# Kernel tuning notes

Hardware: AMD Instinct MI355X
Metric: run time of the kernel (lower is better)

The kernel has to match this reference:

```python
import jax, jax.numpy as jnp
import numpy as np

N = 100000
E = 1600000
DIN = 128
DOUT = 128
NUM_STEPS = 3


def setup_inputs() -> dict:
    key = jax.random.key(0)
    ks = jax.random.split(key, 12)
    stdv = 1.0 / np.sqrt(DOUT)
    xav = np.sqrt(6.0 / (2 * DOUT + DOUT))  # xavier_uniform for [DOUT, 2*DOUT]
    return {
        "input": jax.random.normal(ks[0], (N, DIN), dtype=jnp.float32),
        "edge_row": jax.random.randint(ks[1], (E,), 0, N, dtype=jnp.int32),
        "edge_col": jax.random.randint(ks[2], (E,), 0, N, dtype=jnp.int32),
        "edge_weight": jax.random.uniform(ks[3], (E,), dtype=jnp.float32),
        "weight": jax.random.uniform(ks[4], (DIN, DOUT), jnp.float32, -stdv, stdv),
        "bias": jax.random.uniform(ks[5], (DOUT,), jnp.float32, -stdv, stdv),
        "candidate_weight": jax.random.uniform(ks[6], (DOUT, DOUT), jnp.float32, -stdv, stdv),
        "ug_W": jax.random.uniform(ks[7], (DOUT, 2 * DOUT), jnp.float32, -xav, xav),
        "ug_b": jnp.zeros((DOUT,), jnp.float32),
        "rg_W": jax.random.uniform(ks[8], (DOUT, 2 * DOUT), jnp.float32, -xav, xav),
        "rg_b": jnp.zeros((DOUT,), jnp.float32),
    }


def reference(input, edge_row, edge_col, edge_weight, weight, bias,
              candidate_weight, ug_W, ug_b, rg_W, rg_b):
    n = input.shape[0]
    # h = input @ W + b
    h = input @ weight + bias
    for _ in range(NUM_STEPS):
        # spmm: m[dst] += w_e * h[src]
        msg = edge_weight[:, None] * h[edge_col]          # [E, DOUT]
        m = jax.ops.segment_sum(msg, edge_row, num_segments=n)  # [N, DOUT]
        g = jnp.concatenate([h, m], axis=1)               # [N, 2*DOUT]
        z = jax.nn.sigmoid(g @ ug_W.T + ug_b)
        r = jax.nn.sigmoid(g @ rg_W.T + rg_b)
        cand = jnp.tanh((r * h) @ candidate_weight)
        h = z * h + (1.0 - z) * cand
    return h
```

## Files before the change

kernel.cpp:

```cpp
#include <hip/hip_runtime.h>
#include <math.h>

#define NN 100000
#define EE 1600000
#define D 128
#define NB 782
#define SBLK 392
#define EPB 4096
#define EMAX 2048

typedef __attribute__((ext_vector_type(8))) short short8;
typedef __attribute__((ext_vector_type(4))) float floatx4;

static __device__ __forceinline__ unsigned short f2bf(float f) {
  unsigned int u = __builtin_bit_cast(unsigned int, f);
  u = (u + 0x7fff + ((u >> 16) & 1)) >> 16;
  return (unsigned short)u;
}
static __device__ __forceinline__ unsigned int pk2(float a, float b) {
  return (unsigned int)f2bf(a) | ((unsigned int)f2bf(b) << 16);
}
static __device__ __forceinline__ float bflo(unsigned int u) { return __builtin_bit_cast(float, u << 16); }
static __device__ __forceinline__ float bfhi(unsigned int u) { return __builtin_bit_cast(float, u & 0xffff0000u); }
static __device__ __forceinline__ float bf2f(unsigned short s) {
  return __builtin_bit_cast(float, (unsigned int)s << 16);
}
static __device__ __forceinline__ float sig_f(float x) { return 1.f / (1.f + __expf(-x)); }
static __device__ __forceinline__ float tanh_f(float x) {
  float e = __expf(2.f * x);
  return 1.f - 2.f / (e + 1.f);
}
static __device__ __forceinline__ void fma8(float* acc, float w, uint4 h) {
  acc[0] += w * bflo(h.x); acc[1] += w * bfhi(h.x);
  acc[2] += w * bflo(h.y); acc[3] += w * bfhi(h.y);
  acc[4] += w * bflo(h.z); acc[5] += w * bfhi(h.z);
  acc[6] += w * bflo(h.w); acc[7] += w * bfhi(h.w);
}


__global__ __launch_bounds__(256) void b_count(const int* __restrict__ erow, int* __restrict__ cnt_pb) {
  __shared__ int s[NB];
  const int tid = threadIdx.x;
  for (int b = tid; b < NB; b += 256) s[b] = 0;
  __syncthreads();
  const int base = blockIdx.x * EPB;
#pragma unroll
  for (int i = 0; i < 16; ++i) {
    int idx = base + i * 256 + tid;
    if (idx < EE) atomicAdd(&s[erow[idx] >> 7], 1);
  }
  __syncthreads();
  for (int b = tid; b < NB; b += 256) cnt_pb[blockIdx.x * NB + b] = s[b];
}

__global__ __launch_bounds__(1024) void b_scan(const int* __restrict__ cnt_pb,
                                               int* __restrict__ base_pb, int* __restrict__ bucket_off) {
  __shared__ int s[1024];
  const int b = threadIdx.x;
  int tot = 0;
  if (b < NB) {
    for (int j = 0; j < SBLK; ++j) tot += cnt_pb[j * NB + b];
  }
  s[b] = tot;
  __syncthreads();
  for (int d = 1; d < 1024; d <<= 1) {
    int v = (b >= d) ? s[b - d] : 0;
    __syncthreads();
    s[b] += v;
    __syncthreads();
  }
  int excl = s[b] - tot;
  if (b < NB) {
    bucket_off[b] = excl;
    int run = excl;
    for (int j = 0; j < SBLK; ++j) { base_pb[j * NB + b] = run; run += cnt_pb[j * NB + b]; }
  }
  if (b == NB - 1) bucket_off[NB] = excl + tot;
}

__global__ __launch_bounds__(256) void b_scatter(const int* __restrict__ erow, const int* __restrict__ ecol,
                                                  const float* __restrict__ ew,
                                                  const int* __restrict__ base_pb, int2* __restrict__ arena) {
  __shared__ int cur[NB];
  const int tid = threadIdx.x;
  for (int b = tid; b < NB; b += 256) cur[b] = base_pb[blockIdx.x * NB + b];
  __syncthreads();
  const int base = blockIdx.x * EPB;
#pragma unroll
  for (int i = 0; i < 16; ++i) {
    int idx = base + i * 256 + tid;
    if (idx < EE) {
      int r = erow[idx];
      int pos = atomicAdd(&cur[r >> 7], 1);
      int2 v;
      v.x = ecol[idx] | ((r & 127) << 24);
      v.y = __builtin_bit_cast(int, ew[idx]);
      arena[pos] = v;
    }
  }
}

__global__ __launch_bounds__(256) void b_sort(const int* __restrict__ bucket_off, const int2* __restrict__ arena,
                                              int2* __restrict__ edata, int* __restrict__ row_start) {
  __shared__ int rcnt[128];
  __shared__ int rcur[128];
  const int b = blockIdx.x;
  const int tid = threadIdx.x;
  const int lo = bucket_off[b], hi = bucket_off[b + 1];

  if (tid < 128) rcnt[tid] = 0;
  __syncthreads();
  for (int i = lo + tid; i < hi; i += 256) atomicAdd(&rcnt[(arena[i].x >> 24) & 127], 1);
  __syncthreads();
  int myc = (tid < 128) ? rcnt[tid] : 0;
  for (int d = 1; d < 128; d <<= 1) {
    int v = (tid < 128 && tid >= d) ? rcnt[tid - d] : 0;
    __syncthreads();
    if (tid < 128) rcnt[tid] += v;
    __syncthreads();
  }
  if (tid < 128) {
    int excl = rcnt[tid] - myc;
    rcur[tid] = lo + excl;
    int gr = b * 128 + tid;
    if (gr < NN) row_start[gr] = lo + excl;
  }
  if (b == NB - 1 && tid == 0) row_start[NN] = hi;
  __syncthreads();

  for (int i = lo + tid; i < hi; i += 256) {
    int2 v = arena[i];
    int rl = (v.x >> 24) & 127;
    int pos = atomicAdd(&rcur[rl], 1);
    int2 o;
    o.x = v.x & 0x00FFFFFF;
    o.y = v.y;
    edata[pos] = o;
  }
}

__global__ __launch_bounds__(64) void k_pack_zr(const float* __restrict__ ugW, const float* __restrict__ rgW,
                                                unsigned int* __restrict__ packZR) {
  int g = blockIdx.x;
  int nt = g >> 3, ks = g & 7;
  int lane = threadIdx.x;
  int o = nt * 16 + (lane & 15);
  int c0 = ks * 32 + (lane >> 4) * 8;
  const float* src = (o < 128 ? ugW + (size_t)o * 256 : rgW + (size_t)(o - 128) * 256) + c0;
  float4 f0 = ((const float4*)src)[0];
  float4 f1 = ((const float4*)src)[1];
  uint4 out;
  out.x = pk2(f0.x, f0.y);
  out.y = pk2(f0.z, f0.w);
  out.z = pk2(f1.x, f1.y);
  out.w = pk2(f1.z, f1.w);
  ((uint4*)packZR)[g * 64 + lane] = out;
}

__global__ __launch_bounds__(64) void k_pack_kn(const float* __restrict__ M, unsigned int* __restrict__ pack) {
  int g = blockIdx.x;
  int nt = g >> 2, ks = g & 3;
  int lane = threadIdx.x;
  int n = nt * 16 + (lane & 15);
  int k0 = ks * 32 + (lane >> 4) * 8;
  unsigned short v[8];
#pragma unroll
  for (int j = 0; j < 8; ++j) v[j] = f2bf(M[(size_t)(k0 + j) * 128 + n]);
  uint4 out;
  out.x = (unsigned int)v[0] | ((unsigned int)v[1] << 16);
  out.y = (unsigned int)v[2] | ((unsigned int)v[3] << 16);
  out.z = (unsigned int)v[4] | ((unsigned int)v[5] << 16);
  out.w = (unsigned int)v[6] | ((unsigned int)v[7] << 16);
  ((uint4*)pack)[g * 64 + lane] = out;
}

__global__ __launch_bounds__(256) void init_mfma(
    const float* __restrict__ X, const short* __restrict__ packW, const float* __restrict__ bias,
    unsigned short* __restrict__ h_bf) {
  __shared__ __align__(16) short sX[32 * 136];
  const int tid = threadIdx.x;
  const int row0 = blockIdx.x * 32;

  {
    int r = tid >> 3, ch = tid & 7;
    const float4* px = (const float4*)(X + (size_t)(row0 + r) * D + ch * 16);
    float4 f0 = px[0], f1 = px[1], f2 = px[2], f3 = px[3];
    uint4 o0, o1;
    o0.x = pk2(f0.x, f0.y); o0.y = pk2(f0.z, f0.w);
    o0.z = pk2(f1.x, f1.y); o0.w = pk2(f1.z, f1.w);
    o1.x = pk2(f2.x, f2.y); o1.y = pk2(f2.z, f2.w);
    o1.z = pk2(f3.x, f3.y); o1.w = pk2(f3.z, f3.w);
    *(uint4*)(sX + r * 136 + ch * 16) = o0;
    *(uint4*)(sX + r * 136 + ch * 16 + 8) = o1;
  }
  __syncthreads();

  const int wave = tid >> 6, lane = tid & 63;
  const int quad = lane >> 4, l15 = lane & 15;
  const int mh = wave & 1, nh = wave >> 1;
  const int mrow = mh * 16 + l15;

  floatx4 acc[4];
  const floatx4 zero4 = {0.f, 0.f, 0.f, 0.f};
#pragma unroll
  for (int t = 0; t < 4; ++t) acc[t] = zero4;

  const short8* pW = (const short8*)packW;
#pragma unroll
  for (int ks = 0; ks < 4; ++ks) {
    short8 a = *(const short8*)(sX + mrow * 136 + ks * 32 + quad * 8);
#pragma unroll
    for (int t = 0; t < 4; ++t) {
      short8 b = pW[((nh * 4 + t) * 4 + ks) * 64 + lane];
      acc[t] = __builtin_amdgcn_mfma_f32_16x16x32_bf16(a, b, acc[t], 0, 0, 0);
    }
  }

  __syncthreads();
#pragma unroll
  for (int t = 0; t < 4; ++t) {
    int col = nh * 64 + t * 16 + l15;
    float bv = bias[col];
#pragma unroll
    for (int reg = 0; reg < 4; ++reg) {
      int row = mh * 16 + quad * 4 + reg;
      sX[row * 136 + col] = (short)f2bf(acc[t][reg] + bv);
    }
  }
  __syncthreads();
  for (int idx = tid; idx < 512; idx += 256) {
    int r = idx >> 4, ch = idx & 15;
    *(uint4*)(h_bf + (size_t)(row0 + r) * D + ch * 8) = *(uint4*)(sX + r * 136 + ch * 8);
  }
}

__global__ __launch_bounds__(512, 8) void fused_step(
    const int* __restrict__ row_start, const int2* __restrict__ edata,
    const uint4* __restrict__ h4,
    const short* __restrict__ packZR, const short* __restrict__ packCW,
    const float* __restrict__ ugb, const float* __restrict__ rgb,
    unsigned short* __restrict__ h_bf_out, float* __restrict__ h_f32_out, int last) {
  __shared__ __align__(16) short sA[32 * 264];
  __shared__ __align__(16) char sU[EMAX * 8];
  int2* sE = (int2*)sU;
  short* sRH = (short*)sU;

  const int tid = threadIdx.x;
  const int row0 = blockIdx.x * 32;
  const int wave = tid >> 6, lane = tid & 63;
  const int sub = lane >> 4, li = lane & 15;

  {
    int r = tid >> 4, ch = tid & 15;
    *(uint4*)(sA + r * 264 + ch * 8) = h4[(size_t)(row0 + r) * 16 + ch];
  }

  const int myrow = row0 + wave * 4 + sub;
  const int rs0 = row_start[myrow];
  const int rs1 = row_start[myrow + 1];
  const int seg_lo = row_start[row0];
  const int seg_hi = row_start[row0 + 32];

  float acc[8];
#pragma unroll
  for (int j = 0; j < 8; ++j) acc[j] = 0.f;

  for (int clo = seg_lo; clo < seg_hi; clo += EMAX) {
    const int chi = min(clo + EMAX, seg_hi);
    for (int i = clo + tid; i < chi; i += 512) sE[i - clo] = edata[i];
    __syncthreads();

    int kb = max(rs0, clo) - clo;
    int ke = min(rs1, chi) - clo;
    for (; kb + 2 <= ke; kb += 2) {
      int2 e0 = sE[kb];
      int2 e1 = sE[kb + 1];
      uint4 h0 = h4[(size_t)e0.x * 16 + li];
      uint4 h1 = h4[(size_t)e1.x * 16 + li];
      fma8(acc, __builtin_bit_cast(float, e0.y), h0);
      fma8(acc, __builtin_bit_cast(float, e1.y), h1);
    }
    if (kb < ke) {
      int2 e0 = sE[kb];
      uint4 h0 = h4[(size_t)e0.x * 16 + li];
      fma8(acc, __builtin_bit_cast(float, e0.y), h0);
    }
    __syncthreads();
  }

  {
    uint4 o;
    o.x = pk2(acc[0], acc[1]);
    o.y = pk2(acc[2], acc[3]);
    o.z = pk2(acc[4], acc[5]);
    o.w = pk2(acc[6], acc[7]);
    *(uint4*)(sA + (wave * 4 + sub) * 264 + 128 + li * 8) = o;
  }
  __syncthreads();

  const int quad = lane >> 4, l15 = lane & 15;
  const int mh = wave >> 2, nh = wave & 3;
  const int mrow = mh * 16 + l15;

  floatx4 accZ[2], accR[2];
  const floatx4 zero4 = {0.f, 0.f, 0.f, 0.f};
#pragma unroll
  for (int t = 0; t < 2; ++t) { accZ[t] = zero4; accR[t] = zero4; }

  const short8* pB = (const short8*)packZR;
#pragma unroll
  for (int ks = 0; ks < 8; ++ks) {
    short8 a = *(const short8*)(sA + mrow * 264 + ks * 32 + quad * 8);
#pragma unroll
    for (int t = 0; t < 2; ++t) {
      short8 bz = pB[((nh * 2 + t) * 8 + ks) * 64 + lane];
      accZ[t] = __builtin_amdgcn_mfma_f32_16x16x32_bf16(a, bz, accZ[t], 0, 0, 0);
      short8 br = pB[((8 + nh * 2 + t) * 8 + ks) * 64 + lane];
      accR[t] = __builtin_amdgcn_mfma_f32_16x16x32_bf16(a, br, accR[t], 0, 0, 0);
    }
  }

#pragma unroll
  for (int t = 0; t < 2; ++t) {
    int col = nh * 32 + t * 16 + l15;
    float zb = ugb[col], rb = rgb[col];
#pragma unroll
    for (int reg = 0; reg < 4; ++reg) {
      int row = mh * 16 + quad * 4 + reg;
      float z = sig_f(accZ[t][reg] + zb);
      float rr = sig_f(accR[t][reg] + rb);
      float hv = bf2f((unsigned short)sA[row * 264 + col]);
      sRH[row * 136 + col] = (short)f2bf(rr * hv);
      accZ[t][reg] = z;
    }
  }
  __syncthreads();

  floatx4 acc2[2];
#pragma unroll
  for (int t = 0; t < 2; ++t) acc2[t] = zero4;

  const short8* pC = (const short8*)packCW;
#pragma unroll
  for (int ks = 0; ks < 4; ++ks) {
    short8 a = *(const short8*)(sRH + mrow * 136 + ks * 32 + quad * 8);
#pragma unroll
    for (int t = 0; t < 2; ++t) {
      short8 b = pC[((nh * 2 + t) * 4 + ks) * 64 + lane];
      acc2[t] = __builtin_amdgcn_mfma_f32_16x16x32_bf16(a, b, acc2[t], 0, 0, 0);
    }
  }

#pragma unroll
  for (int t = 0; t < 2; ++t) {
    int col = nh * 32 + t * 16 + l15;
#pragma unroll
    for (int reg = 0; reg < 4; ++reg) {
      int row = mh * 16 + quad * 4 + reg;
      float cand = tanh_f(acc2[t][reg]);
      float z = accZ[t][reg];
      float hold = bf2f((unsigned short)sA[row * 264 + col]);
      float hn = z * hold + (1.f - z) * cand;
      if (last) h_f32_out[(size_t)(row0 + row) * D + col] = hn;
      else sA[row * 264 + col] = (short)f2bf(hn);
    }
  }
  if (!last) {
    __syncthreads();
    int r = tid >> 4, ch = tid & 15;
    *(uint4*)(h_bf_out + (size_t)(row0 + r) * D + ch * 8) = *(uint4*)(sA + r * 264 + ch * 8);
  }
}

extern "C" void kernel_launch(void* const* d_in, const int* in_sizes, int n_in,
                              void* d_out, int out_size, void* d_ws, size_t ws_size,
                              hipStream_t stream) {
  const float* input = (const float*)d_in[0];
  const int* erow    = (const int*)d_in[1];
  const int* ecol    = (const int*)d_in[2];
  const float* ew    = (const float*)d_in[3];
  const float* W     = (const float*)d_in[4];
  const float* bias  = (const float*)d_in[5];
  const float* CW    = (const float*)d_in[6];
  const float* ugW   = (const float*)d_in[7];
  const float* ugb   = (const float*)d_in[8];
  const float* rgW   = (const float*)d_in[9];
  const float* rgb   = (const float*)d_in[10];

  float* h_out = (float*)d_out;

  char* ws = (char*)d_ws;
  unsigned short* hA = (unsigned short*)ws;   ws += (size_t)NN * D * 2;
  unsigned short* hB = (unsigned short*)ws;   ws += (size_t)NN * D * 2;
  unsigned int* packZR = (unsigned int*)ws;   ws += 16 * 8 * 64 * 16;
  unsigned int* packCW = (unsigned int*)ws;   ws += 8 * 4 * 64 * 16;
  unsigned int* packW  = (unsigned int*)ws;   ws += 8 * 4 * 64 * 16;
  int2* arena    = (int2*)ws;                 ws += (size_t)EE * sizeof(int2);
  int2* edata    = (int2*)ws;                 ws += (size_t)EE * sizeof(int2);
  int* bucket_off= (int*)ws;                  ws += (NB + 1) * sizeof(int);
  int* row_start = (int*)ws;                  ws += (NN + 1) * sizeof(int);
  int* cnt_pb  = (int*)hA;
  int* base_pb = (int*)((char*)hA + (size_t)SBLK * NB * sizeof(int));

  b_count<<<SBLK, 256, 0, stream>>>(erow, cnt_pb);
  b_scan<<<1, 1024, 0, stream>>>(cnt_pb, base_pb, bucket_off);
  b_scatter<<<SBLK, 256, 0, stream>>>(erow, ecol, ew, base_pb, arena);
  b_sort<<<NB, 256, 0, stream>>>(bucket_off, arena, edata, row_start);

  k_pack_zr<<<128, 64, 0, stream>>>(ugW, rgW, packZR);
  k_pack_kn<<<32, 64, 0, stream>>>(CW, packCW);
  k_pack_kn<<<32, 64, 0, stream>>>(W, packW);
  init_mfma<<<NN / 32, 256, 0, stream>>>(input, (const short*)packW, bias, hA);

  fused_step<<<NN / 32, 512, 0, stream>>>(row_start, edata, (const uint4*)hA,
                                          (const short*)packZR, (const short*)packCW,
                                          ugb, rgb, hB, h_out, 0);
  fused_step<<<NN / 32, 512, 0, stream>>>(row_start, edata, (const uint4*)hB,
                                          (const short*)packZR, (const short*)packCW,
                                          ugb, rgb, hA, h_out, 0);
  fused_step<<<NN / 32, 512, 0, stream>>>(row_start, edata, (const uint4*)hA,
                                          (const short*)packZR, (const short*)packCW,
                                          ugb, rgb, hB, h_out, 1);
}
```

Baseline: 530.3 us.

## Replace two-level bucket sort CSR build with global atomic count/scan/scatter

Builds the CSR from edges by counting per row with global atomics, a three-stage scan, and scattering edges directly with per-row atomic cursors. This removes the bucket arena pass and the per-bucket local sort kernel, and the three weight-packing kernels are merged into one launch. In exchange, global atomics now contend on 100k rows, and the edge order within each row becomes nondeterministic. That changes the floating-point summation order and gives a less coalesced scatter.

```diff
diff --git a/kernel.cpp b/kernel.cpp
--- a/kernel.cpp
+++ b/kernel.cpp
@@ -4,9 +4,6 @@
 #define NN 100000
 #define EE 1600000
 #define D 128
-#define NB 782
-#define SBLK 392
-#define EPB 4096
 #define EMAX 2048
 
 typedef __attribute__((ext_vector_type(8))) short short8;
@@ -38,140 +35,106 @@
 }
 
 
-__global__ __launch_bounds__(256) void b_count(const int* __restrict__ erow, int* __restrict__ cnt_pb) {
-  __shared__ int s[NB];
-  const int tid = threadIdx.x;
-  for (int b = tid; b < NB; b += 256) s[b] = 0;
-  __syncthreads();
-  const int base = blockIdx.x * EPB;
-#pragma unroll
-  for (int i = 0; i < 16; ++i) {
-    int idx = base + i * 256 + tid;
-    if (idx < EE) atomicAdd(&s[erow[idx] >> 7], 1);
-  }
-  __syncthreads();
-  for (int b = tid; b < NB; b += 256) cnt_pb[blockIdx.x * NB + b] = s[b];
-}
-
-__global__ __launch_bounds__(1024) void b_scan(const int* __restrict__ cnt_pb,
-                                               int* __restrict__ base_pb, int* __restrict__ bucket_off) {
+__global__ __launch_bounds__(256) void r_count(const int* __restrict__ erow, int* __restrict__ cnt) {
+  int idx = blockIdx.x * 256 + threadIdx.x;
+  if (idx < EE) atomicAdd(&cnt[erow[idx]], 1);
+}
+
+__global__ __launch_bounds__(1024) void r_scan1(const int* __restrict__ cnt,
+                                                int* __restrict__ row_start, int* __restrict__ bsum) {
   __shared__ int s[1024];
-  const int b = threadIdx.x;
-  int tot = 0;
-  if (b < NB) {
-    for (int j = 0; j < SBLK; ++j) tot += cnt_pb[j * NB + b];
-  }
-  s[b] = tot;
+  const int t = threadIdx.x;
+  const int idx = blockIdx.x * 1024 + t;
+  int v = (idx < NN) ? cnt[idx] : 0;
+  s[t] = v;
   __syncthreads();
   for (int d = 1; d < 1024; d <<= 1) {
-    int v = (b >= d) ? s[b - d] : 0;
-    __syncthreads();
-    s[b] += v;
-    __syncthreads();
-  }
-  int excl = s[b] - tot;
-  if (b < NB) {
-    bucket_off[b] = excl;
-    int run = excl;
-    for (int j = 0; j < SBLK; ++j) { base_pb[j * NB + b] = run; run += cnt_pb[j * NB + b]; }
-  }
-  if (b == NB - 1) bucket_off[NB] = excl + tot;
-}
-
-__global__ __launch_bounds__(256) void b_scatter(const int* __restrict__ erow, const int* __restrict__ ecol,
-                                                  const float* __restrict__ ew,
-                                                  const int* __restrict__ base_pb, int2* __restrict__ arena) {
-  __shared__ int cur[NB];
-  const int tid = threadIdx.x;
-  for (int b = tid; b < NB; b += 256) cur[b] = base_pb[blockIdx.x * NB + b];
-  __syncthreads();
-  const int base = blockIdx.x * EPB;
-#pragma unroll
-  for (int i = 0; i < 16; ++i) {
-    int idx = base + i * 256 + tid;
-    if (idx < EE) {
-      int r = erow[idx];
-      int pos = atomicAdd(&cur[r >> 7], 1);
-      int2 v;
-      v.x = ecol[idx] | ((r & 127) << 24);
-      v.y = __builtin_bit_cast(int, ew[idx]);
-      arena[pos] = v;
-    }
-  }
-}
-
-__global__ __launch_bounds__(256) void b_sort(const int* __restrict__ bucket_off, const int2* __restrict__ arena,
-                                              int2* __restrict__ edata, int* __restrict__ row_start) {
-  __shared__ int rcnt[128];
-  __shared__ int rcur[128];
-  const int b = blockIdx.x;
-  const int tid = threadIdx.x;
-  const int lo = bucket_off[b], hi = bucket_off[b + 1];
-
-  if (tid < 128) rcnt[tid] = 0;
-  __syncthreads();
-  for (int i = lo + tid; i < hi; i += 256) atomicAdd(&rcnt[(arena[i].x >> 24) & 127], 1);
-  __syncthreads();
-  int myc = (tid < 128) ? rcnt[tid] : 0;
+    int x = (t >= d) ? s[t - d] : 0;
+    __syncthreads();
+    s[t] += x;
+    __syncthreads();
+  }
+  if (idx < NN) row_start[idx] = s[t] - v;
+  if (t == 1023) bsum[blockIdx.x] = s[1023];
+}
+
+__global__ __launch_bounds__(128) void r_scan2(int* __restrict__ bsum) {
+  __shared__ int s[128];
+  const int t = threadIdx.x;
+  int v = (t < 98) ? bsum[t] : 0;
+  s[t] = v;
+  __syncthreads();
   for (int d = 1; d < 128; d <<= 1) {
-    int v = (tid < 128 && tid >= d) ? rcnt[tid - d] : 0;
-    __syncthreads();
-    if (tid < 128) rcnt[tid] += v;
-    __syncthreads();
-  }
-  if (tid < 128) {
-    int excl = rcnt[tid] - myc;
-    rcur[tid] = lo + excl;
-    int gr = b * 128 + tid;
-    if (gr < NN) row_start[gr] = lo + excl;
-  }
-  if (b == NB - 1 && tid == 0) row_start[NN] = hi;
-  __syncthreads();
-
-  for (int i = lo + tid; i < hi; i += 256) {
-    int2 v = arena[i];
-    int rl = (v.x >> 24) & 127;
-    int pos = atomicAdd(&rcur[rl], 1);
-    int2 o;
-    o.x = v.x & 0x00FFFFFF;
-    o.y = v.y;
-    edata[pos] = o;
-  }
-}
-
-__global__ __launch_bounds__(64) void k_pack_zr(const float* __restrict__ ugW, const float* __restrict__ rgW,
-                                                unsigned int* __restrict__ packZR) {
-  int g = blockIdx.x;
-  int nt = g >> 3, ks = g & 7;
+    int x = (t >= d) ? s[t - d] : 0;
+    __syncthreads();
+    s[t] += x;
+    __syncthreads();
+  }
+  if (t < 98) bsum[t] = s[t] - v;
+}
+
+__global__ __launch_bounds__(1024) void r_scan3(int* __restrict__ row_start, int* __restrict__ row_cur,
+                                                const int* __restrict__ bsum) {
+  const int idx = blockIdx.x * 1024 + threadIdx.x;
+  if (idx < NN) {
+    int v = row_start[idx] + bsum[blockIdx.x];
+    row_start[idx] = v;
+    row_cur[idx] = v;
+  }
+  if (blockIdx.x == 0 && threadIdx.x == 0) row_start[NN] = EE;
+}
+
+__global__ __launch_bounds__(256) void r_scatter(const int* __restrict__ erow, const int* __restrict__ ecol,
+                                                 const float* __restrict__ ew,
+                                                 int* __restrict__ row_cur, int2* __restrict__ edata) {
+  int idx = blockIdx.x * 256 + threadIdx.x;
+  if (idx < EE) {
+    int r = erow[idx];
+    int pos = atomicAdd(&row_cur[r], 1);
+    int2 v;
+    v.x = ecol[idx];
+    v.y = __builtin_bit_cast(int, ew[idx]);
+    edata[pos] = v;
+  }
+}
+
+__global__ __launch_bounds__(64) void k_pack_all(const float* __restrict__ ugW, const float* __restrict__ rgW,
+                                                 const float* __restrict__ CW, const float* __restrict__ W,
+                                                 unsigned int* __restrict__ packZR,
+                                                 unsigned int* __restrict__ packCW,
+                                                 unsigned int* __restrict__ packW) {
   int lane = threadIdx.x;
-  int o = nt * 16 + (lane & 15);
-  int c0 = ks * 32 + (lane >> 4) * 8;
-  const float* src = (o < 128 ? ugW + (size_t)o * 256 : rgW + (size_t)(o - 128) * 256) + c0;
-  float4 f0 = ((const float4*)src)[0];
-  float4 f1 = ((const float4*)src)[1];
-  uint4 out;
-  out.x = pk2(f0.x, f0.y);
-  out.y = pk2(f0.z, f0.w);
-  out.z = pk2(f1.x, f1.y);
-  out.w = pk2(f1.z, f1.w);
-  ((uint4*)packZR)[g * 64 + lane] = out;
-}
-
-__global__ __launch_bounds__(64) void k_pack_kn(const float* __restrict__ M, unsigned int* __restrict__ pack) {
-  int g = blockIdx.x;
-  int nt = g >> 2, ks = g & 3;
-  int lane = threadIdx.x;
-  int n = nt * 16 + (lane & 15);
-  int k0 = ks * 32 + (lane >> 4) * 8;
-  unsigned short v[8];
-#pragma unroll
-  for (int j = 0; j < 8; ++j) v[j] = f2bf(M[(size_t)(k0 + j) * 128 + n]);
-  uint4 out;
-  out.x = (unsigned int)v[0] | ((unsigned int)v[1] << 16);
-  out.y = (unsigned int)v[2] | ((unsigned int)v[3] << 16);
-  out.z = (unsigned int)v[4] | ((unsigned int)v[5] << 16);
-  out.w = (unsigned int)v[6] | ((unsigned int)v[7] << 16);
-  ((uint4*)pack)[g * 64 + lane] = out;
+  if (blockIdx.x < 128) {
+    int g = blockIdx.x;
+    int nt = g >> 3, ks = g & 7;
+    int o = nt * 16 + (lane & 15);
+    int c0 = ks * 32 + (lane >> 4) * 8;
+    const float* src = (o < 128 ? ugW + (size_t)o * 256 : rgW + (size_t)(o - 128) * 256) + c0;
+    float4 f0 = ((const float4*)src)[0];
+    float4 f1 = ((const float4*)src)[1];
+    uint4 out;
+    out.x = pk2(f0.x, f0.y);
+    out.y = pk2(f0.z, f0.w);
+    out.z = pk2(f1.x, f1.y);
+    out.w = pk2(f1.z, f1.w);
+    ((uint4*)packZR)[g * 64 + lane] = out;
+  } else {
+    const float* M = (blockIdx.x < 160) ? CW : W;
+    unsigned int* dst = (blockIdx.x < 160) ? packCW : packW;
+    int g = (blockIdx.x - 128) & 31;
+    int nt = g >> 2, ks = g & 3;
+    int n = nt * 16 + (lane & 15);
+    int k0 = ks * 32 + (lane >> 4) * 8;
+    unsigned short v[8];
+#pragma unroll
+    for (int j = 0; j < 8; ++j) v[j] = f2bf(M[(size_t)(k0 + j) * 128 + n]);
+    uint4 out;
+    out.x = (unsigned int)v[0] | ((unsigned int)v[1] << 16);
+    out.y = (unsigned int)v[2] | ((unsigned int)v[3] << 16);
+    out.z = (unsigned int)v[4] | ((unsigned int)v[5] << 16);
+    out.w = (unsigned int)v[6] | ((unsigned int)v[7] << 16);
+    ((uint4*)dst)[g * 64 + lane] = out;
+  }
 }
 
 __global__ __launch_bounds__(256) void init_mfma(
@@ -395,21 +358,20 @@
   unsigned int* packZR = (unsigned int*)ws;   ws += 16 * 8 * 64 * 16;
   unsigned int* packCW = (unsigned int*)ws;   ws += 8 * 4 * 64 * 16;
   unsigned int* packW  = (unsigned int*)ws;   ws += 8 * 4 * 64 * 16;
-  int2* arena    = (int2*)ws;                 ws += (size_t)EE * sizeof(int2);
   int2* edata    = (int2*)ws;                 ws += (size_t)EE * sizeof(int2);
-  int* bucket_off= (int*)ws;                  ws += (NB + 1) * sizeof(int);
+  int* row_cnt   = (int*)ws;                  ws += NN * sizeof(int);
   int* row_start = (int*)ws;                  ws += (NN + 1) * sizeof(int);
-  int* cnt_pb  = (int*)hA;
-  int* base_pb = (int*)((char*)hA + (size_t)SBLK * NB * sizeof(int));
-
-  b_count<<<SBLK, 256, 0, stream>>>(erow, cnt_pb);
-  b_scan<<<1, 1024, 0, stream>>>(cnt_pb, base_pb, bucket_off);
-  b_scatter<<<SBLK, 256, 0, stream>>>(erow, ecol, ew, base_pb, arena);
-  b_sort<<<NB, 256, 0, stream>>>(bucket_off, arena, edata, row_start);
-
-  k_pack_zr<<<128, 64, 0, stream>>>(ugW, rgW, packZR);
-  k_pack_kn<<<32, 64, 0, stream>>>(CW, packCW);
-  k_pack_kn<<<32, 64, 0, stream>>>(W, packW);
+  int* row_cur   = (int*)ws;                  ws += NN * sizeof(int);
+  int* bsum      = (int*)ws;                  ws += 128 * sizeof(int);
+
+  hipMemsetAsync(row_cnt, 0, (size_t)NN * sizeof(int), stream);
+  r_count<<<(EE + 255) / 256, 256, 0, stream>>>(erow, row_cnt);
+  r_scan1<<<98, 1024, 0, stream>>>(row_cnt, row_start, bsum);
+  r_scan2<<<1, 128, 0, stream>>>(bsum);
+  r_scan3<<<98, 1024, 0, stream>>>(row_start, row_cur, bsum);
+  r_scatter<<<(EE + 255) / 256, 256, 0, stream>>>(erow, ecol, ew, row_cur, edata);
+
+  k_pack_all<<<192, 64, 0, stream>>>(ugW, rgW, CW, W, packZR, packCW, packW);
   init_mfma<<<NN / 32, 256, 0, stream>>>(input, (const short*)packW, bias, hA);
 
   fused_step<<<NN / 32, 512, 0, stream>>>(row_start, edata, (const uint4*)hA,
```

Result: slower. 617.6 us (+16.5%).

## Replace per-block bucket scan with global atomic bucket counts and merge pack kernels

Applied to the files above, without the earlier changes.

The edge bucketing preprocessing now uses global atomics for per-bucket totals instead of a per-block count matrix. That removes the single-block scan's serial loops over 392 blocks per bucket. Scatter blocks reserve their ranges with one atomic per bucket, after a local count in shared memory. Larger 1024-thread blocks now cover 16K edges each, and the three weight-pack kernels are merged into a single launch. In exchange the order of edges within a bucket depends on atomics, so floating-point summation order is not deterministic, and a memset launch is added.

```diff
diff --git a/kernel.cpp b/kernel.cpp
--- a/kernel.cpp
+++ b/kernel.cpp
@@ -4,9 +4,9 @@
 #define NN 100000
 #define EE 1600000
 #define D 128
-#define NB 782
-#define SBLK 392
-#define EPB 4096
+#define NBK 782
+#define SBLK 98
+#define EPB 16384
 #define EMAX 2048
 
 typedef __attribute__((ext_vector_type(8))) short short8;
@@ -38,62 +38,67 @@
 }
 
 
-__global__ __launch_bounds__(256) void b_count(const int* __restrict__ erow, int* __restrict__ cnt_pb) {
-  __shared__ int s[NB];
+__global__ __launch_bounds__(1024) void b_count(const int* __restrict__ erow, int* __restrict__ bucket_tot) {
+  __shared__ int s[NBK];
   const int tid = threadIdx.x;
-  for (int b = tid; b < NB; b += 256) s[b] = 0;
+  for (int b = tid; b < NBK; b += 1024) s[b] = 0;
   __syncthreads();
   const int base = blockIdx.x * EPB;
 #pragma unroll
   for (int i = 0; i < 16; ++i) {
-    int idx = base + i * 256 + tid;
+    int idx = base + i * 1024 + tid;
     if (idx < EE) atomicAdd(&s[erow[idx] >> 7], 1);
   }
   __syncthreads();
-  for (int b = tid; b < NB; b += 256) cnt_pb[blockIdx.x * NB + b] = s[b];
-}
-
-__global__ __launch_bounds__(1024) void b_scan(const int* __restrict__ cnt_pb,
-                                               int* __restrict__ base_pb, int* __restrict__ bucket_off) {
+  for (int b = tid; b < NBK; b += 1024) if (s[b]) atomicAdd(&bucket_tot[b], s[b]);
+}
+
+__global__ __launch_bounds__(1024) void b_off(const int* __restrict__ bucket_tot,
+                                              int* __restrict__ bucket_off, int* __restrict__ bucket_cur) {
   __shared__ int s[1024];
-  const int b = threadIdx.x;
-  int tot = 0;
-  if (b < NB) {
-    for (int j = 0; j < SBLK; ++j) tot += cnt_pb[j * NB + b];
-  }
-  s[b] = tot;
+  const int t = threadIdx.x;
+  int v = (t < NBK) ? bucket_tot[t] : 0;
+  s[t] = v;
   __syncthreads();
   for (int d = 1; d < 1024; d <<= 1) {
-    int v = (b >= d) ? s[b - d] : 0;
-    __syncthreads();
-    s[b] += v;
-    __syncthreads();
-  }
-  int excl = s[b] - tot;
-  if (b < NB) {
-    bucket_off[b] = excl;
-    int run = excl;
-    for (int j = 0; j < SBLK; ++j) { base_pb[j * NB + b] = run; run += cnt_pb[j * NB + b]; }
-  }
-  if (b == NB - 1) bucket_off[NB] = excl + tot;
-}
-
-__global__ __launch_bounds__(256) void b_scatter(const int* __restrict__ erow, const int* __restrict__ ecol,
+    int x = (t >= d) ? s[t - d] : 0;
+    __syncthreads();
+    s[t] += x;
+    __syncthreads();
+  }
+  int excl = s[t] - v;
+  if (t < NBK) { bucket_off[t] = excl; bucket_cur[t] = excl; }
+  if (t == NBK - 1) bucket_off[NBK] = excl + v;
+}
+
+__global__ __launch_bounds__(1024) void b_scatter(const int* __restrict__ erow, const int* __restrict__ ecol,
                                                   const float* __restrict__ ew,
-                                                  const int* __restrict__ base_pb, int2* __restrict__ arena) {
-  __shared__ int cur[NB];
+                                                  int* __restrict__ bucket_cur, int2* __restrict__ arena) {
+  __shared__ int cur[NBK];
   const int tid = threadIdx.x;
-  for (int b = tid; b < NB; b += 256) cur[b] = base_pb[blockIdx.x * NB + b];
+  for (int b = tid; b < NBK; b += 1024) cur[b] = 0;
   __syncthreads();
   const int base = blockIdx.x * EPB;
+  int r[16];
 #pragma unroll
   for (int i = 0; i < 16; ++i) {
-    int idx = base + i * 256 + tid;
-    if (idx < EE) {
-      int r = erow[idx];
-      int pos = atomicAdd(&cur[r >> 7], 1);
+    int idx = base + i * 1024 + tid;
+    r[i] = (idx < EE) ? erow[idx] : -1;
+    if (r[i] >= 0) atomicAdd(&cur[r[i] >> 7], 1);
+  }
+  __syncthreads();
+  for (int b = tid; b < NBK; b += 1024) {
+    int c = cur[b];
+    cur[b] = c ? atomicAdd(&bucket_cur[b], c) : 0;
+  }
+  __syncthreads();
+#pragma unroll
+  for (int i = 0; i < 16; ++i) {
+    if (r[i] >= 0) {
+      int idx = base + i * 1024 + tid;
+      int pos = atomicAdd(&cur[r[i] >> 7], 1);
       int2 v;
-      v.x = ecol[idx] | ((r & 127) << 24);
+      v.x = ecol[idx] | ((r[i] & 127) << 24);
       v.y = __builtin_bit_cast(int, ew[idx]);
       arena[pos] = v;
     }
@@ -125,7 +130,7 @@
     int gr = b * 128 + tid;
     if (gr < NN) row_start[gr] = lo + excl;
   }
-  if (b == NB - 1 && tid == 0) row_start[NN] = hi;
+  if (b == NBK - 1 && tid == 0) row_start[NN] = hi;
   __syncthreads();
 
   for (int i = lo + tid; i < hi; i += 256) {
@@ -139,39 +144,43 @@
   }
 }
 
-__global__ __launch_bounds__(64) void k_pack_zr(const float* __restrict__ ugW, const float* __restrict__ rgW,
-                                                unsigned int* __restrict__ packZR) {
-  int g = blockIdx.x;
-  int nt = g >> 3, ks = g & 7;
+__global__ __launch_bounds__(64) void k_pack_all(const float* __restrict__ ugW, const float* __restrict__ rgW,
+                                                 const float* __restrict__ CW, const float* __restrict__ W,
+                                                 unsigned int* __restrict__ packZR,
+                                                 unsigned int* __restrict__ packCW,
+                                                 unsigned int* __restrict__ packW) {
   int lane = threadIdx.x;
-  int o = nt * 16 + (lane & 15);
-  int c0 = ks * 32 + (lane >> 4) * 8;
-  const float* src = (o < 128 ? ugW + (size_t)o * 256 : rgW + (size_t)(o - 128) * 256) + c0;
-  float4 f0 = ((const float4*)src)[0];
-  float4 f1 = ((const float4*)src)[1];
-  uint4 out;
-  out.x = pk2(f0.x, f0.y);
-  out.y = pk2(f0.z, f0.w);
-  out.z = pk2(f1.x, f1.y);
-  out.w = pk2(f1.z, f1.w);
-  ((uint4*)packZR)[g * 64 + lane] = out;
-}
-
-__global__ __launch_bounds__(64) void k_pack_kn(const float* __restrict__ M, unsigned int* __restrict__ pack) {
-  int g = blockIdx.x;
-  int nt = g >> 2, ks = g & 3;
-  int lane = threadIdx.x;
-  int n = nt * 16 + (lane & 15);
-  int k0 = ks * 32 + (lane >> 4) * 8;
-  unsigned short v[8];
-#pragma unroll
-  for (int j = 0; j < 8; ++j) v[j] = f2bf(M[(size_t)(k0 + j) * 128 + n]);
-  uint4 out;
-  out.x = (unsigned int)v[0] | ((unsigned int)v[1] << 16);
-  out.y = (unsigned int)v[2] | ((unsigned int)v[3] << 16);
-  out.z = (unsigned int)v[4] | ((unsigned int)v[5] << 16);
-  out.w = (unsigned int)v[6] | ((unsigned int)v[7] << 16);
-  ((uint4*)pack)[g * 64 + lane] = out;
+  if (blockIdx.x < 128) {
+    int g = blockIdx.x;
+    int nt = g >> 3, ks = g & 7;
+    int o = nt * 16 + (lane & 15);
+    int c0 = ks * 32 + (lane >> 4) * 8;
+    const float* src = (o < 128 ? ugW + (size_t)o * 256 : rgW + (size_t)(o - 128) * 256) + c0;
+    float4 f0 = ((const float4*)src)[0];
+    float4 f1 = ((const float4*)src)[1];
+    uint4 out;
+    out.x = pk2(f0.x, f0.y);
+    out.y = pk2(f0.z, f0.w);
+    out.z = pk2(f1.x, f1.y);
+    out.w = pk2(f1.z, f1.w);
+    ((uint4*)packZR)[g * 64 + lane] = out;
+  } else {
+    const float* M = (blockIdx.x < 160) ? CW : W;
+    unsigned int* dst = (blockIdx.x < 160) ? packCW : packW;
+    int g = (blockIdx.x - 128) & 31;
+    int nt = g >> 2, ks = g & 3;
+    int n = nt * 16 + (lane & 15);
+    int k0 = ks * 32 + (lane >> 4) * 8;
+    unsigned short v[8];
+#pragma unroll
+    for (int j = 0; j < 8; ++j) v[j] = f2bf(M[(size_t)(k0 + j) * 128 + n]);
+    uint4 out;
+    out.x = (unsigned int)v[0] | ((unsigned int)v[1] << 16);
+    out.y = (unsigned int)v[2] | ((unsigned int)v[3] << 16);
+    out.z = (unsigned int)v[4] | ((unsigned int)v[5] << 16);
+    out.w = (unsigned int)v[6] | ((unsigned int)v[7] << 16);
+    ((uint4*)dst)[g * 64 + lane] = out;
+  }
 }
 
 __global__ __launch_bounds__(256) void init_mfma(
@@ -397,19 +406,18 @@
   unsigned int* packW  = (unsigned int*)ws;   ws += 8 * 4 * 64 * 16;
   int2* arena    = (int2*)ws;                 ws += (size_t)EE * sizeof(int2);
   int2* edata    = (int2*)ws;                 ws += (size_t)EE * sizeof(int2);
-  int* bucket_off= (int*)ws;                  ws += (NB + 1) * sizeof(int);
+  int* bucket_tot= (int*)ws;                  ws += NBK * sizeof(int);
+  int* bucket_off= (int*)ws;                  ws += (NBK + 1) * sizeof(int);
+  int* bucket_cur= (int*)ws;                  ws += NBK * sizeof(int);
   int* row_start = (int*)ws;                  ws += (NN + 1) * sizeof(int);
-  int* cnt_pb  = (int*)hA;
-  int* base_pb = (int*)((char*)hA + (size_t)SBLK * NB * sizeof(int));
-
-  b_count<<<SBLK, 256, 0, stream>>>(erow, cnt_pb);
-  b_scan<<<1, 1024, 0, stream>>>(cnt_pb, base_pb, bucket_off);
-  b_scatter<<<SBLK, 256, 0, stream>>>(erow, ecol, ew, base_pb, arena);
-  b_sort<<<NB, 256, 0, stream>>>(bucket_off, arena, edata, row_start);
-
-  k_pack_zr<<<128, 64, 0, stream>>>(ugW, rgW, packZR);
-  k_pack_kn<<<32, 64, 0, stream>>>(CW, packCW);
-  k_pack_kn<<<32, 64, 0, stream>>>(W, packW);
+
+  hipMemsetAsync(bucket_tot, 0, NBK * sizeof(int), stream);
+  b_count<<<SBLK, 1024, 0, stream>>>(erow, bucket_tot);
+  b_off<<<1, 1024, 0, stream>>>(bucket_tot, bucket_off, bucket_cur);
+  b_scatter<<<SBLK, 1024, 0, stream>>>(erow, ecol, ew, bucket_cur, arena);
+  b_sort<<<NBK, 256, 0, stream>>>(bucket_off, arena, edata, row_start);
+
+  k_pack_all<<<192, 64, 0, stream>>>(ugW, rgW, CW, W, packZR, packCW, packW);
   init_mfma<<<NN / 32, 256, 0, stream>>>(input, (const short*)packW, bias, hA);
 
   fused_step<<<NN / 32, 512, 0, stream>>>(row_start, edata, (const uint4*)hA,
```

Measured after the change: 495.9 us. 6.5% less time.
